# Optimization experiments

Measured on AMD Instinct MI355X. Metric: run time of the kernel, lower is better.

## Reference

```python
import jax, jax.numpy as jnp
import numpy as np

N_GRAPHS = 1250
NEG_SLOPE = 0.2

def gat_layer(x, src, dst, W, a_src, a_dst, b, concat):
    # x: [N, Fin]; W: [Fin, H*C]; a_src/a_dst: [H, C]; b: [H*C] or [C]
    N = x.shape[0]
    H, C = a_src.shape
    h = (x @ W).reshape(N, H, C)                      # [N,H,C]
    alpha_s = jnp.sum(h * a_src[None], axis=-1)       # [N,H]
    alpha_d = jnp.sum(h * a_dst[None], axis=-1)       # [N,H]
    e = jax.nn.leaky_relu(alpha_s[src] + alpha_d[dst], NEG_SLOPE)  # [E,H]
    # segment softmax over incoming edges of each target node
    m = jax.ops.segment_max(e, dst, num_segments=N)   # [N,H]
    m = jnp.where(jnp.isfinite(m), m, 0.0)
    ex = jnp.exp(e - m[dst])
    s = jax.ops.segment_sum(ex, dst, num_segments=N)  # [N,H]
    alpha = ex / (s[dst] + 1e-16)                     # [E,H]
    msg = h[src] * alpha[..., None]                   # [E,H,C]
    out = jax.ops.segment_sum(msg, dst, num_segments=N)  # [N,H,C]
    out = out.reshape(N, H * C) if concat else out.mean(axis=1)
    return out + b

def setup_inputs() -> dict:
    key = jax.random.key(0)
    ks = jax.random.split(key, 13)
    N, E = 50000, 100000
    x = jax.random.normal(ks[0], (N, 78), dtype=jnp.float32)
    edge_index = jax.random.randint(ks[1], (2, E), 0, N, dtype=jnp.int64)
    # sorted segment ids -> every graph non-empty (~40 nodes each)
    batch = jnp.sort(jax.random.randint(ks[2], (N,), 0, N_GRAPHS, dtype=jnp.int64))
    g = lambda k, shape, fan: jax.random.normal(k, shape, dtype=jnp.float32) / np.float32(np.sqrt(fan))
    return {
        'x': x, 'edge_index': edge_index, 'batch': batch,
        'W1': g(ks[3], (78, 780), 78), 'a_src1': g(ks[4], (10, 78), 78), 'a_dst1': g(ks[5], (10, 78), 78),
        'b1': jnp.zeros((780,), jnp.float32),
        'W2': g(ks[6], (780, 128), 780), 'a_src2': g(ks[7], (1, 128), 128), 'a_dst2': g(ks[8], (1, 128), 128),
        'b2': jnp.zeros((128,), jnp.float32),
        'fc_w': g(ks[9], (128, 128), 128), 'fc_b': jnp.zeros((128,), jnp.float32),
    }

def reference(x, edge_index, batch, W1, a_src1, a_dst1, b1, W2, a_src2, a_dst2, b2, fc_w, fc_b):
    N = x.shape[0]
    loop = jnp.arange(N, dtype=edge_index.dtype)
    src = jnp.concatenate([edge_index[0], loop])  # add self loops (PyG default)
    dst = jnp.concatenate([edge_index[1], loop])
    # dropout layers are identity in eval mode
    h = jax.nn.elu(gat_layer(x, src, dst, W1, a_src1, a_dst1, b1, concat=True))   # [N,780]
    h = jax.nn.relu(gat_layer(h, src, dst, W2, a_src2, a_dst2, b2, concat=True))  # [N,128]
    g = jax.ops.segment_max(h, batch, num_segments=N_GRAPHS)                      # [G,128]
    g = jnp.where(jnp.isfinite(g), g, 0.0)
    return jax.nn.relu(g @ fc_w + fc_b)
```

## Files before the change

kernel.cpp:

```cpp
#include <hip/hip_runtime.h>
#include <hip/hip_bf16.h>
#include <cstdint>

#define CAP 32
typedef __hip_bfloat16 bf16;
typedef __attribute__((ext_vector_type(8))) short short8;
typedef __attribute__((ext_vector_type(4))) float f32x4;

__device__ __forceinline__ float sb2f(short s) {
  unsigned int u = ((unsigned int)(unsigned short)s) << 16;
  return __uint_as_float(u);
}
__device__ __forceinline__ short f2sb(float f) {
  bf16 h = __float2bfloat16(f);
  return *reinterpret_cast<short*>(&h);
}

__global__ void k_zero(float* __restrict__ p, int n) {
  int i = blockIdx.x * 256 + threadIdx.x;
  if (i < n) p[i] = 0.f;
}

__global__ void k_detect(const int* __restrict__ ei, int* __restrict__ flag) {
  __shared__ int any;
  if (threadIdx.x == 0) any = 0;
  __syncthreads();
  int v = 0;
  for (int i = 1 + 2 * threadIdx.x; i < 2000; i += 512) v |= ei[i];
  if (v) atomicOr(&any, 1);
  __syncthreads();
  if (threadIdx.x == 0) flag[0] = (any == 0) ? 1 : 0;
}

__device__ __forceinline__ void edge_sd(const int* __restrict__ ei, int e, int f,
                                        int& src, int& dst) {
  if (e < 100000) {
    if (f) { src = ei[2 * e]; dst = ei[200000 + 2 * e]; }
    else   { src = ei[e];     dst = ei[100000 + e]; }
  } else { src = dst = e - 100000; }
  src = min(max(src, 0), 49999);
  dst = min(max(dst, 0), 49999);
}

__global__ void k_prep(const float* __restrict__ x, const float* __restrict__ W1,
                       const float* __restrict__ W2, const float* __restrict__ aw1,
                       const float* __restrict__ dw1, bf16* __restrict__ xb,
                       bf16* __restrict__ W1t, bf16* __restrict__ W2t,
                       bf16* __restrict__ Wat) {
  int i = blockIdx.x * 256 + threadIdx.x;
  const int n_xb = 50000 * 96;
  const int n_w1 = 832 * 96;
  const int n_w2 = 128 * 832;
  const int n_wa = 32 * 96;
  if (i < n_xb) {
    int r = i / 96, k = i - r * 96;
    xb[i] = __float2bfloat16(k < 78 ? x[r * 78 + k] : 0.f);
  } else if (i < n_xb + n_w1) {
    int j = i - n_xb;
    int n = j / 96, k = j - n * 96;
    W1t[j] = __float2bfloat16((k < 78 && n < 780) ? W1[k * 780 + n] : 0.f);
  } else if (i < n_xb + n_w1 + n_w2) {
    int j = i - n_xb - n_w1;
    int c = j / 832, k = j - c * 832;
    W2t[j] = __float2bfloat16(k < 780 ? W2[k * 128 + c] : 0.f);
  } else if (i < n_xb + n_w1 + n_w2 + n_wa) {
    int j = i - n_xb - n_w1 - n_w2;
    int c = j / 96, k = j - c * 96;
    float s = 0.f;
    if (k < 78 && c < 20) {
      const float* w = (c < 10) ? aw1 : dw1;
      int h = (c < 10) ? c : c - 10;
      const float* wrow = W1 + k * 780 + h * 78;
      const float* arow = w + h * 78;
      for (int q = 0; q < 78; q++) s += wrow[q] * arow[q];
    }
    Wat[c * 96 + k] = __float2bfloat16(s);
  }
}

__global__ __launch_bounds__(256) void k_gemm1(const bf16* __restrict__ xb,
                                               const bf16* __restrict__ W1t,
                                               const bf16* __restrict__ Wat,
                                               bf16* __restrict__ H1,
                                               float* __restrict__ as1,
                                               float* __restrict__ ad1) {
  __shared__ __align__(16) short Als[64 * 104];
  __shared__ __align__(16) short Bls[64 * 104];
  __shared__ __align__(16) short Wls[32 * 104];
  const int t = threadIdx.x;
  const int w = t >> 6, l = t & 63, l15 = l & 15, q = l >> 4;
  const int rowBase = blockIdx.x * 64;
  for (int s = t; s < 768; s += 256) {
    int row = s / 12, kg = s - row * 12;
    short8 v = {};
    int gr = rowBase + row;
    if (gr < 50000) v = *(const short8*)((const short*)xb + (size_t)gr * 96 + kg * 8);
    *(short8*)&Als[row * 104 + kg * 8] = v;
  }
  for (int s = t; s < 384; s += 256) {
    int row = s / 12, kg = s - row * 12;
    short8 v = *(const short8*)((const short*)Wat + (size_t)row * 96 + kg * 8);
    *(short8*)&Wls[row * 104 + kg * 8] = v;
  }
  for (int cc = 0; cc < 13; cc++) {
    __syncthreads();
    for (int s = t; s < 768; s += 256) {
      int n = s / 12, kg = s - n * 12;
      short8 v = *(const short8*)((const short*)W1t + (size_t)(cc * 64 + n) * 96 + kg * 8);
      *(short8*)&Bls[n * 104 + kg * 8] = v;
    }
    __syncthreads();
    f32x4 acc[4] = {};
#pragma unroll
    for (int ks = 0; ks < 3; ks++) {
      short8 a = *(const short8*)&Als[(w * 16 + l15) * 104 + ks * 32 + q * 8];
#pragma unroll
      for (int nt = 0; nt < 4; nt++) {
        short8 b = *(const short8*)&Bls[(nt * 16 + l15) * 104 + ks * 32 + q * 8];
        acc[nt] = __builtin_amdgcn_mfma_f32_16x16x32_bf16(a, b, acc[nt], 0, 0, 0);
      }
    }
    const int gr0 = rowBase + w * 16 + q * 4;
#pragma unroll
    for (int nt = 0; nt < 4; nt++) {
      int gc = cc * 64 + nt * 16 + l15;
#pragma unroll
      for (int r = 0; r < 4; r++) {
        int gr = gr0 + r;
        if (gr < 50000) H1[(size_t)gr * 832 + gc] = __float2bfloat16(acc[nt][r]);
      }
    }
  }
  f32x4 acc2[2] = {};
#pragma unroll
  for (int ks = 0; ks < 3; ks++) {
    short8 a = *(const short8*)&Als[(w * 16 + l15) * 104 + ks * 32 + q * 8];
#pragma unroll
    for (int nt = 0; nt < 2; nt++) {
      short8 b = *(const short8*)&Wls[(nt * 16 + l15) * 104 + ks * 32 + q * 8];
      acc2[nt] = __builtin_amdgcn_mfma_f32_16x16x32_bf16(a, b, acc2[nt], 0, 0, 0);
    }
  }
  const int gr0 = rowBase + w * 16 + q * 4;
#pragma unroll
  for (int nt = 0; nt < 2; nt++) {
    int c = nt * 16 + l15;
#pragma unroll
    for (int r = 0; r < 4; r++) {
      int gr = gr0 + r;
      if (gr < 50000) {
        if (c < 10)       as1[gr * 10 + c] = acc2[nt][r];
        else if (c < 20)  ad1[gr * 10 + (c - 10)] = acc2[nt][r];
      }
    }
  }
}

__global__ void k_scatter(const int* __restrict__ ei, const int* __restrict__ flag,
                          int* __restrict__ cnt, int* __restrict__ csr) {
  int e = blockIdx.x * 256 + threadIdx.x;
  if (e >= 150000) return;
  int f = flag[0], src, dst;
  edge_sd(ei, e, f, src, dst);
  int pos = atomicAdd(&cnt[dst], 1);
  if (pos < CAP) csr[dst * CAP + pos] = src;
}

__global__ __launch_bounds__(256) void k_agg1(const bf16* __restrict__ H1,
                                              const float* __restrict__ as1,
                                              const float* __restrict__ ad1,
                                              const int* __restrict__ csr,
                                              const int* __restrict__ cnt,
                                              const float* __restrict__ b1,
                                              bf16* __restrict__ HL2) {
  __shared__ float sexw[2][CAP * 10];
  __shared__ float sden[2][16];
  __shared__ float b1p[832];
  __shared__ int ssrc[2][CAP];
  __shared__ int scnt[2];
  const int t = threadIdx.x;
  const int sub = t >> 7, tt = t & 127;
  const int n = blockIdx.x * 2 + sub;
  if (t < 2) scnt[t] = min(cnt[blockIdx.x * 2 + t], CAP);
  if (t >= 32 && t < 64) { int z = t - 32; sden[z >> 4][z & 15] = 0.f; }
  for (int i = t; i < 832; i += 256) b1p[i] = (i < 780) ? b1[i] : 0.f;
  __syncthreads();
  const int cn = scnt[sub];
  if (tt < cn) ssrc[sub][tt] = csr[n * CAP + tt];
  __syncthreads();
  for (int wv = tt; wv < cn * 10; wv += 128) {
    int k = wv / 10, h = wv - k * 10;
    int src = ssrc[sub][k];
    float e = as1[src * 10 + h] + ad1[n * 10 + h];
    e = e >= 0.f ? e : 0.2f * e;
    float ex = __expf(e);
    sexw[sub][wv] = ex;
    atomicAdd(&sden[sub][h], ex);
  }
  __syncthreads();
  for (int wv = tt; wv < cn * 10; wv += 128) {
    int h = wv % 10;
    sexw[sub][wv] = sexw[sub][wv] / (sden[sub][h] + 1e-16f);
  }
  __syncthreads();
  if (tt < 104) {
    int hj[8];
#pragma unroll
    for (int c = 0; c < 8; c++) {
      int j = tt * 8 + c;
      int h = j / 78;
      hj[c] = h > 9 ? 9 : h;
    }
    float acc[8] = {};
    const float* sw = sexw[sub];
    const short* H1s = (const short*)H1;
    for (int k = 0; k < cn; k++) {
      int src = ssrc[sub][k];
      short8 hv = *(const short8*)(H1s + (size_t)src * 832 + tt * 8);
      const float* swk = sw + k * 10;
#pragma unroll
      for (int c = 0; c < 8; c++) acc[c] += swk[hj[c]] * sb2f(hv[c]);
    }
    short8 ov;
#pragma unroll
    for (int c = 0; c < 8; c++) {
      int j = tt * 8 + c;
      float v = acc[c] + b1p[j];
      v = v > 0.f ? v : __expf(v) - 1.f;
      ov[c] = f2sb(v);
    }
    *(short8*)((short*)HL2 + (size_t)n * 832 + tt * 8) = ov;
  }
}

__global__ __launch_bounds__(256) void k_gemm2(const bf16* __restrict__ A,
                                               const bf16* __restrict__ W2t,
                                               const float* __restrict__ AW2,
                                               const float* __restrict__ DW2,
                                               bf16* __restrict__ H2,
                                               float* __restrict__ as2,
                                               float* __restrict__ ad2) {
  __shared__ __align__(16) short Als[64 * 72];
  __shared__ __align__(16) short Bls[128 * 72];
  __shared__ float sAW[128], sDW[128];
  __shared__ float sS[4][64], sD[4][64];
  const int t = threadIdx.x;
  const int w = t >> 6, l = t & 63, l15 = l & 15, q = l >> 4;
  const int rowBase = blockIdx.x * 64;
  if (t < 128) sAW[t] = AW2[t];
  else         sDW[t - 128] = DW2[t - 128];
  f32x4 acc[4][2] = {};
  for (int kb = 0; kb < 832; kb += 64) {
    __syncthreads();
    for (int s = t; s < 512; s += 256) {
      int row = s >> 3, kg = s & 7;
      short8 v = {};
      int gr = rowBase + row;
      if (gr < 50000) v = *(const short8*)((const short*)A + (size_t)gr * 832 + kb + kg * 8);
      *(short8*)&Als[row * 72 + kg * 8] = v;
    }
    for (int s = t; s < 1024; s += 256) {
      int col = s >> 3, kg = s & 7;
      short8 v = *(const short8*)((const short*)W2t + (size_t)col * 832 + kb + kg * 8);
      *(short8*)&Bls[col * 72 + kg * 8] = v;
    }
    __syncthreads();
#pragma unroll
    for (int ks = 0; ks < 2; ks++) {
      short8 a[4];
#pragma unroll
      for (int mt = 0; mt < 4; mt++)
        a[mt] = *(const short8*)&Als[(mt * 16 + l15) * 72 + ks * 32 + q * 8];
#pragma unroll
      for (int ntl = 0; ntl < 2; ntl++) {
        short8 b = *(const short8*)&Bls[((w * 2 + ntl) * 16 + l15) * 72 + ks * 32 + q * 8];
#pragma unroll
        for (int mt = 0; mt < 4; mt++)
          acc[mt][ntl] = __builtin_amdgcn_mfma_f32_16x16x32_bf16(a[mt], b, acc[mt][ntl], 0, 0, 0);
      }
    }
  }
  const int col0 = w * 32 + l15, col1 = col0 + 16;
  const float aw0 = sAW[col0], aw1 = sAW[col1];
  const float dw0 = sDW[col0], dw1 = sDW[col1];
  f32x4 sp[4], dp[4];
#pragma unroll
  for (int mt = 0; mt < 4; mt++) {
    sp[mt] = acc[mt][0] * aw0 + acc[mt][1] * aw1;
    dp[mt] = acc[mt][0] * dw0 + acc[mt][1] * dw1;
  }
#pragma unroll
  for (int m = 1; m < 16; m <<= 1) {
#pragma unroll
    for (int mt = 0; mt < 4; mt++)
#pragma unroll
      for (int r = 0; r < 4; r++) {
        sp[mt][r] += __shfl_xor(sp[mt][r], m, 64);
        dp[mt][r] += __shfl_xor(dp[mt][r], m, 64);
      }
  }
  if (l15 == 0) {
#pragma unroll
    for (int mt = 0; mt < 4; mt++)
#pragma unroll
      for (int r = 0; r < 4; r++) {
        sS[w][mt * 16 + q * 4 + r] = sp[mt][r];
        sD[w][mt * 16 + q * 4 + r] = dp[mt][r];
      }
  }
#pragma unroll
  for (int mt = 0; mt < 4; mt++) {
    int gr0 = rowBase + mt * 16 + q * 4;
#pragma unroll
    for (int ntl = 0; ntl < 2; ntl++) {
      int gc = w * 32 + ntl * 16 + l15;
#pragma unroll
      for (int r = 0; r < 4; r++) {
        int gr = gr0 + r;
        if (gr < 50000) H2[(size_t)gr * 128 + gc] = __float2bfloat16(acc[mt][ntl][r]);
      }
    }
  }
  __syncthreads();
  if (t < 64) {
    int gr = rowBase + t;
    if (gr < 50000) as2[gr] = sS[0][t] + sS[1][t] + sS[2][t] + sS[3][t];
  } else if (t < 128) {
    int r2 = t - 64;
    int gr = rowBase + r2;
    if (gr < 50000) ad2[gr] = sD[0][r2] + sD[1][r2] + sD[2][r2] + sD[3][r2];
  }
}

__global__ __launch_bounds__(256) void k_agg2(const bf16* __restrict__ H2,
                                              const float* __restrict__ as2,
                                              const float* __restrict__ ad2,
                                              const int* __restrict__ csr,
                                              const int* __restrict__ cnt,
                                              const float* __restrict__ b2,
                                              const int* __restrict__ batch,
                                              const int* __restrict__ flag,
                                              float* __restrict__ g) {
  __shared__ int ssrc[2][CAP];
  __shared__ float sexw[2][CAP];
  __shared__ float sden[2];
  __shared__ int scnt[2], sb[2];
  const int t = threadIdx.x;
  const int sub = t >> 7, tt = t & 127;
  const int n = blockIdx.x * 2 + sub;
  if (t < 2) {
    int nt2 = blockIdx.x * 2 + t;
    scnt[t] = min(cnt[nt2], CAP);
    sden[t] = 0.f;
    int b = flag[0] ? batch[2 * nt2] : batch[nt2];
    sb[t] = min(max(b, 0), 1249);
  }
  __syncthreads();
  const int cn = scnt[sub];
  if (tt < cn) {
    int src = csr[n * CAP + tt];
    ssrc[sub][tt] = src;
    float e = as2[src] + ad2[n];
    e = e >= 0.f ? e : 0.2f * e;
    float ex = __expf(e);
    sexw[sub][tt] = ex;
    atomicAdd(&sden[sub], ex);
  }
  __syncthreads();
  if (tt < cn) sexw[sub][tt] = sexw[sub][tt] / (sden[sub] + 1e-16f);
  __syncthreads();
  const short* H2s = (const short*)H2;
  float acc = 0.f;
  for (int k = 0; k < cn; k++)
    acc += sexw[sub][k] * sb2f(H2s[(size_t)ssrc[sub][k] * 128 + tt]);
  float v = acc + b2[tt];
  v = v > 0.f ? v : 0.f;
  atomicMax((int*)&g[sb[sub] * 128 + tt], __float_as_int(v));
}

__global__ __launch_bounds__(128) void k_fc(const float* __restrict__ g,
                                            const float* __restrict__ fw,
                                            const float* __restrict__ fb,
                                            float* __restrict__ out) {
  const int n = blockIdx.x, t = threadIdx.x;
  __shared__ float grow[128];
  grow[t] = g[n * 128 + t];
  __syncthreads();
  float acc = fb[t];
  for (int k = 0; k < 128; k++) acc += grow[k] * fw[k * 128 + t];
  out[n * 128 + t] = acc > 0.f ? acc : 0.f;
}

extern "C" void kernel_launch(void* const* d_in, const int* in_sizes, int n_in,
                              void* d_out, int out_size, void* d_ws, size_t ws_size,
                              hipStream_t stream) {
  const float* x     = (const float*)d_in[0];
  const int*   ei    = (const int*)d_in[1];
  const int*   batch = (const int*)d_in[2];
  const float* W1    = (const float*)d_in[3];
  const float* as1w  = (const float*)d_in[4];
  const float* ad1w  = (const float*)d_in[5];
  const float* b1    = (const float*)d_in[6];
  const float* W2    = (const float*)d_in[7];
  const float* as2w  = (const float*)d_in[8];
  const float* ad2w  = (const float*)d_in[9];
  const float* b2    = (const float*)d_in[10];
  const float* fcw   = (const float*)d_in[11];
  const float* fcb   = (const float*)d_in[12];
  float* out = (float*)d_out;

  char* p = (char*)d_ws;
  size_t off = 0;
  auto alloc = [&](size_t bytes) -> void* {
    void* r = p + off;
    off = (off + bytes + 15) & ~(size_t)15;
    return r;
  };
  int*   cnt = (int*)  alloc(50000 * 4);
  float* g   = (float*)alloc(160000 * 4);
  size_t zeroWords = off / 4;
  float* as1 = (float*)alloc(500000 * 4);
  float* ad1 = (float*)alloc(500000 * 4);
  float* as2 = (float*)alloc(50000 * 4);
  float* ad2 = (float*)alloc(50000 * 4);
  bf16*  W1t = (bf16*) alloc((size_t)832 * 96 * 2);
  bf16*  W2t = (bf16*) alloc((size_t)128 * 832 * 2);
  bf16*  Wat = (bf16*) alloc((size_t)32 * 96 * 2);
  bf16*  h1  = (bf16*) alloc((size_t)50000 * 832 * 2);
  bf16*  hl2 = (bf16*) alloc((size_t)50000 * 832 * 2);
  int*   csr = (int*)  alloc((size_t)50000 * CAP * 4);
  void*  uni = alloc((size_t)50000 * 128 * 2);
  bf16*  xb  = (bf16*)uni;
  bf16*  h2  = (bf16*)uni;
  int*   flag = (int*) alloc(16);
  (void)ws_size; (void)in_sizes; (void)n_in; (void)out_size;

  k_zero<<<((int)zeroWords + 255) / 256, 256, 0, stream>>>((float*)d_ws, (int)zeroWords);
  k_detect<<<1, 256, 0, stream>>>(ei, flag);
  k_prep<<<(50000 * 96 + 832 * 96 + 128 * 832 + 32 * 96 + 255) / 256, 256, 0, stream>>>(
      x, W1, W2, as1w, ad1w, xb, W1t, W2t, Wat);

  k_gemm1<<<782, 256, 0, stream>>>(xb, W1t, Wat, h1, as1, ad1);
  k_scatter<<<(150000 + 255) / 256, 256, 0, stream>>>(ei, flag, cnt, csr);
  k_agg1<<<25000, 256, 0, stream>>>(h1, as1, ad1, csr, cnt, b1, hl2);
  k_gemm2<<<782, 256, 0, stream>>>(hl2, W2t, as2w, ad2w, h2, as2, ad2);
  k_agg2<<<25000, 256, 0, stream>>>(h2, as2, ad2, csr, cnt, b2, batch, flag, g);
  k_fc<<<1250, 128, 0, stream>>>(g, fcw, fcb, out);
}
```

Before: 320.6 us.

## Prefetch GEMM tiles into registers, stage GEMM1 output via LDS, fold zeroing into prep

Both GEMM kernels now load the next K or N tile from global memory into registers while the current tile is computed, so global latency overlaps with MFMA work. GEMM1 writes its accumulator tile to shared memory first and then stores H1 with coalesced 16-byte bf16 rows instead of scattered 2-byte stores. The separate zeroing kernel is merged into the prep kernel, removing one launch. This costs extra registers and LDS (a 17 KB fp32 staging buffer) plus two extra barriers per chunk, which may lower occupancy. The merge also relies on the prep grid covering at least as many threads as there are words to zero.

```diff
diff --git a/kernel.cpp b/kernel.cpp
--- a/kernel.cpp
+++ b/kernel.cpp
@@ -14,11 +14,6 @@
 __device__ __forceinline__ short f2sb(float f) {
   bf16 h = __float2bfloat16(f);
   return *reinterpret_cast<short*>(&h);
-}
-
-__global__ void k_zero(float* __restrict__ p, int n) {
-  int i = blockIdx.x * 256 + threadIdx.x;
-  if (i < n) p[i] = 0.f;
 }
 
 __global__ void k_detect(const int* __restrict__ ei, int* __restrict__ flag) {
@@ -46,8 +41,9 @@
                        const float* __restrict__ W2, const float* __restrict__ aw1,
                        const float* __restrict__ dw1, bf16* __restrict__ xb,
                        bf16* __restrict__ W1t, bf16* __restrict__ W2t,
-                       bf16* __restrict__ Wat) {
+                       bf16* __restrict__ Wat, float* __restrict__ zp, int zeroWords) {
   int i = blockIdx.x * 256 + threadIdx.x;
+  if (i < zeroWords) zp[i] = 0.f;
   const int n_xb = 50000 * 96;
   const int n_w1 = 832 * 96;
   const int n_w2 = 128 * 832;
@@ -87,6 +83,7 @@
   __shared__ __align__(16) short Als[64 * 104];
   __shared__ __align__(16) short Bls[64 * 104];
   __shared__ __align__(16) short Wls[32 * 104];
+  __shared__ __align__(16) float Cls[64 * 68];
   const int t = threadIdx.x;
   const int w = t >> 6, l = t & 63, l15 = l & 15, q = l >> 4;
   const int rowBase = blockIdx.x * 64;
@@ -99,15 +96,26 @@
   }
   for (int s = t; s < 384; s += 256) {
     int row = s / 12, kg = s - row * 12;
-    short8 v = *(const short8*)((const short*)Wat + (size_t)row * 96 + kg * 8);
-    *(short8*)&Wls[row * 104 + kg * 8] = v;
+    *(short8*)&Wls[row * 104 + kg * 8] =
+        *(const short8*)((const short*)Wat + (size_t)row * 96 + kg * 8);
+  }
+  short8 breg[3];
+  int bn[3], bk[3];
+#pragma unroll
+  for (int i = 0; i < 3; i++) {
+    int s = t + i * 256;
+    bn[i] = s / 12; bk[i] = s - bn[i] * 12;
+    breg[i] = *(const short8*)((const short*)W1t + (size_t)bn[i] * 96 + bk[i] * 8);
   }
   for (int cc = 0; cc < 13; cc++) {
     __syncthreads();
-    for (int s = t; s < 768; s += 256) {
-      int n = s / 12, kg = s - n * 12;
-      short8 v = *(const short8*)((const short*)W1t + (size_t)(cc * 64 + n) * 96 + kg * 8);
-      *(short8*)&Bls[n * 104 + kg * 8] = v;
+#pragma unroll
+    for (int i = 0; i < 3; i++) *(short8*)&Bls[bn[i] * 104 + bk[i] * 8] = breg[i];
+    if (cc < 12) {
+#pragma unroll
+      for (int i = 0; i < 3; i++)
+        breg[i] = *(const short8*)((const short*)W1t +
+                                   (size_t)((cc + 1) * 64 + bn[i]) * 96 + bk[i] * 8);
     }
     __syncthreads();
     f32x4 acc[4] = {};
@@ -120,14 +128,25 @@
         acc[nt] = __builtin_amdgcn_mfma_f32_16x16x32_bf16(a, b, acc[nt], 0, 0, 0);
       }
     }
-    const int gr0 = rowBase + w * 16 + q * 4;
-#pragma unroll
-    for (int nt = 0; nt < 4; nt++) {
-      int gc = cc * 64 + nt * 16 + l15;
-#pragma unroll
-      for (int r = 0; r < 4; r++) {
-        int gr = gr0 + r;
-        if (gr < 50000) H1[(size_t)gr * 832 + gc] = __float2bfloat16(acc[nt][r]);
+    __syncthreads();
+#pragma unroll
+    for (int nt = 0; nt < 4; nt++)
+#pragma unroll
+      for (int r = 0; r < 4; r++)
+        Cls[(w * 16 + q * 4 + r) * 68 + nt * 16 + l15] = acc[nt][r];
+    __syncthreads();
+    {
+      int r = t >> 2, c0 = (t & 3) * 16;
+      int gr = rowBase + r;
+      if (gr < 50000) {
+        short8 o0, o1;
+#pragma unroll
+        for (int c = 0; c < 8; c++) o0[c] = f2sb(Cls[r * 68 + c0 + c]);
+#pragma unroll
+        for (int c = 0; c < 8; c++) o1[c] = f2sb(Cls[r * 68 + c0 + 8 + c]);
+        short* dst = (short*)H1 + (size_t)gr * 832 + cc * 64 + c0;
+        *(short8*)dst = o0;
+        *(short8*)(dst + 8) = o1;
       }
     }
   }
@@ -249,20 +268,54 @@
   const int rowBase = blockIdx.x * 64;
   if (t < 128) sAW[t] = AW2[t];
   else         sDW[t - 128] = DW2[t - 128];
+  const int ar = t >> 2, ak = t & 3;
+  const int bc = t >> 1, bk2 = t & 1;
+  short8 areg[2], breg[4];
+  {
+    int gr0 = rowBase + ar;
+#pragma unroll
+    for (int i = 0; i < 2; i++) {
+      short8 v = {};
+      int gr = gr0;
+      if (gr < 50000)
+        v = *(const short8*)((const short*)A + (size_t)gr * 832 + 0 + (ak * 2 + i) * 8);
+      areg[i] = v;
+    }
+#pragma unroll
+    for (int i = 0; i < 4; i++) {
+      int s = t + i * 256;
+      int col = s >> 3, kg = s & 7;
+      breg[i] = *(const short8*)((const short*)W2t + (size_t)col * 832 + 0 + kg * 8);
+    }
+  }
   f32x4 acc[4][2] = {};
   for (int kb = 0; kb < 832; kb += 64) {
     __syncthreads();
-    for (int s = t; s < 512; s += 256) {
-      int row = s >> 3, kg = s & 7;
-      short8 v = {};
-      int gr = rowBase + row;
-      if (gr < 50000) v = *(const short8*)((const short*)A + (size_t)gr * 832 + kb + kg * 8);
-      *(short8*)&Als[row * 72 + kg * 8] = v;
-    }
-    for (int s = t; s < 1024; s += 256) {
+#pragma unroll
+    for (int i = 0; i < 2; i++)
+      *(short8*)&Als[ar * 72 + (ak * 2 + i) * 8] = areg[i];
+#pragma unroll
+    for (int i = 0; i < 4; i++) {
+      int s = t + i * 256;
       int col = s >> 3, kg = s & 7;
-      short8 v = *(const short8*)((const short*)W2t + (size_t)col * 832 + kb + kg * 8);
-      *(short8*)&Bls[col * 72 + kg * 8] = v;
+      *(short8*)&Bls[col * 72 + kg * 8] = breg[i];
+    }
+    if (kb < 768) {
+      int kn = kb + 64;
+      int gr = rowBase + ar;
+#pragma unroll
+      for (int i = 0; i < 2; i++) {
+        short8 v = {};
+        if (gr < 50000)
+          v = *(const short8*)((const short*)A + (size_t)gr * 832 + kn + (ak * 2 + i) * 8);
+        areg[i] = v;
+      }
+#pragma unroll
+      for (int i = 0; i < 4; i++) {
+        int s = t + i * 256;
+        int col = s >> 3, kg = s & 7;
+        breg[i] = *(const short8*)((const short*)W2t + (size_t)col * 832 + kn + kg * 8);
+      }
     }
     __syncthreads();
 #pragma unroll
@@ -435,10 +488,10 @@
   int*   flag = (int*) alloc(16);
   (void)ws_size; (void)in_sizes; (void)n_in; (void)out_size;
 
-  k_zero<<<((int)zeroWords + 255) / 256, 256, 0, stream>>>((float*)d_ws, (int)zeroWords);
   k_detect<<<1, 256, 0, stream>>>(ei, flag);
-  k_prep<<<(50000 * 96 + 832 * 96 + 128 * 832 + 32 * 96 + 255) / 256, 256, 0, stream>>>(
-      x, W1, W2, as1w, ad1w, xb, W1t, W2t, Wat);
+  int prepN = 50000 * 96 + 832 * 96 + 128 * 832 + 32 * 96;
+  k_prep<<<(prepN + 255) / 256, 256, 0, stream>>>(
+      x, W1, W2, as1w, ad1w, xb, W1t, W2t, Wat, (float*)d_ws, (int)zeroWords);
 
   k_gemm1<<<782, 256, 0, stream>>>(xb, W1t, Wat, h1, as1, ad1);
   k_scatter<<<(150000 + 255) / 256, 256, 0, stream>>>(ei, flag, cnt, csr);
```

Result: faster. 294.2 us (-8.2%).

## Aggregate raw inputs before layer-1 projection and fuse projection into layer-2 GEMM

Applied to the files above, without the earlier changes.

The layer-1 GEMM that materialised the N×780 hidden tensor is dropped. Attention-weighted aggregation now runs on the 78-wide inputs per head, giving a 10×96 aggregate per node. A fused kernel then applies each head's block of W1, the bias and ELU in shared memory, and feeds the result straight into the layer-2 GEMM. This removes a large intermediate write and re-read and shrinks the gather width in aggregation, at the cost of a per-node 10-head aggregate buffer and more MFMA work per GEMM block. Zeroing moves into the prep kernel, and the separate normalisation passes and metadata syncs in the aggregation kernels are removed.

```diff
diff --git a/kernel.cpp b/kernel.cpp
--- a/kernel.cpp
+++ b/kernel.cpp
@@ -14,11 +14,6 @@
 __device__ __forceinline__ short f2sb(float f) {
   bf16 h = __float2bfloat16(f);
   return *reinterpret_cast<short*>(&h);
-}
-
-__global__ void k_zero(float* __restrict__ p, int n) {
-  int i = blockIdx.x * 256 + threadIdx.x;
-  if (i < n) p[i] = 0.f;
 }
 
 __global__ void k_detect(const int* __restrict__ ei, int* __restrict__ flag) {
@@ -45,26 +40,19 @@
 __global__ void k_prep(const float* __restrict__ x, const float* __restrict__ W1,
                        const float* __restrict__ W2, const float* __restrict__ aw1,
                        const float* __restrict__ dw1, bf16* __restrict__ xb,
-                       bf16* __restrict__ W1t, bf16* __restrict__ W2t,
-                       bf16* __restrict__ Wat) {
+                       bf16* __restrict__ Wat, bf16* __restrict__ W1bdp,
+                       bf16* __restrict__ W2h, float* __restrict__ zp, int zeroWords) {
   int i = blockIdx.x * 256 + threadIdx.x;
+  if (i < zeroWords) zp[i] = 0.f;
   const int n_xb = 50000 * 96;
-  const int n_w1 = 832 * 96;
-  const int n_w2 = 128 * 832;
   const int n_wa = 32 * 96;
+  const int n_bd = 10 * 96 * 96;
+  const int n_w2 = 10 * 128 * 96;
   if (i < n_xb) {
     int r = i / 96, k = i - r * 96;
     xb[i] = __float2bfloat16(k < 78 ? x[r * 78 + k] : 0.f);
-  } else if (i < n_xb + n_w1) {
+  } else if (i < n_xb + n_wa) {
     int j = i - n_xb;
-    int n = j / 96, k = j - n * 96;
-    W1t[j] = __float2bfloat16((k < 78 && n < 780) ? W1[k * 780 + n] : 0.f);
-  } else if (i < n_xb + n_w1 + n_w2) {
-    int j = i - n_xb - n_w1;
-    int c = j / 832, k = j - c * 832;
-    W2t[j] = __float2bfloat16(k < 780 ? W2[k * 128 + c] : 0.f);
-  } else if (i < n_xb + n_w1 + n_w2 + n_wa) {
-    int j = i - n_xb - n_w1 - n_w2;
     int c = j / 96, k = j - c * 96;
     float s = 0.f;
     if (k < 78 && c < 20) {
@@ -75,17 +63,26 @@
       for (int q = 0; q < 78; q++) s += wrow[q] * arow[q];
     }
     Wat[c * 96 + k] = __float2bfloat16(s);
-  }
-}
-
-__global__ __launch_bounds__(256) void k_gemm1(const bf16* __restrict__ xb,
-                                               const bf16* __restrict__ W1t,
+  } else if (i < n_xb + n_wa + n_bd) {
+    int j = i - n_xb - n_wa;
+    int hh = j / 9216;
+    int rem = j - hh * 9216;
+    int jj = rem / 96, k = rem - jj * 96;
+    W1bdp[j] = __float2bfloat16((jj < 78 && k < 78) ? W1[k * 780 + hh * 78 + jj] : 0.f);
+  } else if (i < n_xb + n_wa + n_bd + n_w2) {
+    int j = i - n_xb - n_wa - n_bd;
+    int hh = j / 12288;
+    int rem = j - hh * 12288;
+    int c = rem / 96, k = rem - c * 96;
+    W2h[j] = __float2bfloat16(k < 78 ? W2[(hh * 78 + k) * 128 + c] : 0.f);
+  }
+}
+
+__global__ __launch_bounds__(256) void k_alpha(const bf16* __restrict__ xb,
                                                const bf16* __restrict__ Wat,
-                                               bf16* __restrict__ H1,
                                                float* __restrict__ as1,
                                                float* __restrict__ ad1) {
   __shared__ __align__(16) short Als[64 * 104];
-  __shared__ __align__(16) short Bls[64 * 104];
   __shared__ __align__(16) short Wls[32 * 104];
   const int t = threadIdx.x;
   const int w = t >> 6, l = t & 63, l15 = l & 15, q = l >> 4;
@@ -99,38 +96,10 @@
   }
   for (int s = t; s < 384; s += 256) {
     int row = s / 12, kg = s - row * 12;
-    short8 v = *(const short8*)((const short*)Wat + (size_t)row * 96 + kg * 8);
-    *(short8*)&Wls[row * 104 + kg * 8] = v;
-  }
-  for (int cc = 0; cc < 13; cc++) {
-    __syncthreads();
-    for (int s = t; s < 768; s += 256) {
-      int n = s / 12, kg = s - n * 12;
-      short8 v = *(const short8*)((const short*)W1t + (size_t)(cc * 64 + n) * 96 + kg * 8);
-      *(short8*)&Bls[n * 104 + kg * 8] = v;
-    }
-    __syncthreads();
-    f32x4 acc[4] = {};
-#pragma unroll
-    for (int ks = 0; ks < 3; ks++) {
-      short8 a = *(const short8*)&Als[(w * 16 + l15) * 104 + ks * 32 + q * 8];
-#pragma unroll
-      for (int nt = 0; nt < 4; nt++) {
-        short8 b = *(const short8*)&Bls[(nt * 16 + l15) * 104 + ks * 32 + q * 8];
-        acc[nt] = __builtin_amdgcn_mfma_f32_16x16x32_bf16(a, b, acc[nt], 0, 0, 0);
-      }
-    }
-    const int gr0 = rowBase + w * 16 + q * 4;
-#pragma unroll
-    for (int nt = 0; nt < 4; nt++) {
-      int gc = cc * 64 + nt * 16 + l15;
-#pragma unroll
-      for (int r = 0; r < 4; r++) {
-        int gr = gr0 + r;
-        if (gr < 50000) H1[(size_t)gr * 832 + gc] = __float2bfloat16(acc[nt][r]);
-      }
-    }
-  }
+    *(short8*)&Wls[row * 104 + kg * 8] =
+        *(const short8*)((const short*)Wat + (size_t)row * 96 + kg * 8);
+  }
+  __syncthreads();
   f32x4 acc2[2] = {};
 #pragma unroll
   for (int ks = 0; ks < 3; ks++) {
@@ -166,26 +135,20 @@
   if (pos < CAP) csr[dst * CAP + pos] = src;
 }
 
-__global__ __launch_bounds__(256) void k_agg1(const bf16* __restrict__ H1,
+__global__ __launch_bounds__(256) void k_aggx(const bf16* __restrict__ xb,
                                               const float* __restrict__ as1,
                                               const float* __restrict__ ad1,
                                               const int* __restrict__ csr,
                                               const int* __restrict__ cnt,
-                                              const float* __restrict__ b1,
-                                              bf16* __restrict__ HL2) {
+                                              bf16* __restrict__ aggx) {
   __shared__ float sexw[2][CAP * 10];
   __shared__ float sden[2][16];
-  __shared__ float b1p[832];
   __shared__ int ssrc[2][CAP];
-  __shared__ int scnt[2];
   const int t = threadIdx.x;
   const int sub = t >> 7, tt = t & 127;
   const int n = blockIdx.x * 2 + sub;
-  if (t < 2) scnt[t] = min(cnt[blockIdx.x * 2 + t], CAP);
-  if (t >= 32 && t < 64) { int z = t - 32; sden[z >> 4][z & 15] = 0.f; }
-  for (int i = t; i < 832; i += 256) b1p[i] = (i < 780) ? b1[i] : 0.f;
-  __syncthreads();
-  const int cn = scnt[sub];
+  if (tt < 16) sden[sub][tt] = 0.f;
+  const int cn = min(cnt[n], CAP);
   if (tt < cn) ssrc[sub][tt] = csr[n * CAP + tt];
   __syncthreads();
   for (int wv = tt; wv < cn * 10; wv += 128) {
@@ -198,82 +161,102 @@
     atomicAdd(&sden[sub][h], ex);
   }
   __syncthreads();
-  for (int wv = tt; wv < cn * 10; wv += 128) {
-    int h = wv % 10;
-    sexw[sub][wv] = sexw[sub][wv] / (sden[sub][h] + 1e-16f);
-  }
-  __syncthreads();
-  if (tt < 104) {
-    int hj[8];
-#pragma unroll
-    for (int c = 0; c < 8; c++) {
-      int j = tt * 8 + c;
-      int h = j / 78;
-      hj[c] = h > 9 ? 9 : h;
-    }
-    float acc[8] = {};
-    const float* sw = sexw[sub];
-    const short* H1s = (const short*)H1;
+  if (tt < 96) {
+    float acc[10];
+#pragma unroll
+    for (int h = 0; h < 10; h++) acc[h] = 0.f;
+    const short* xs = (const short*)xb;
     for (int k = 0; k < cn; k++) {
       int src = ssrc[sub][k];
-      short8 hv = *(const short8*)(H1s + (size_t)src * 832 + tt * 8);
-      const float* swk = sw + k * 10;
-#pragma unroll
-      for (int c = 0; c < 8; c++) acc[c] += swk[hj[c]] * sb2f(hv[c]);
-    }
-    short8 ov;
-#pragma unroll
-    for (int c = 0; c < 8; c++) {
-      int j = tt * 8 + c;
-      float v = acc[c] + b1p[j];
-      v = v > 0.f ? v : __expf(v) - 1.f;
-      ov[c] = f2sb(v);
-    }
-    *(short8*)((short*)HL2 + (size_t)n * 832 + tt * 8) = ov;
-  }
-}
-
-__global__ __launch_bounds__(256) void k_gemm2(const bf16* __restrict__ A,
-                                               const bf16* __restrict__ W2t,
-                                               const float* __restrict__ AW2,
-                                               const float* __restrict__ DW2,
-                                               bf16* __restrict__ H2,
-                                               float* __restrict__ as2,
-                                               float* __restrict__ ad2) {
-  __shared__ __align__(16) short Als[64 * 72];
-  __shared__ __align__(16) short Bls[128 * 72];
-  __shared__ float sAW[128], sDW[128];
+      float xv = sb2f(xs[(size_t)src * 96 + tt]);
+      const float* swk = sexw[sub] + k * 10;
+#pragma unroll
+      for (int h = 0; h < 10; h++) acc[h] += swk[h] * xv;
+    }
+    short* outp = (short*)aggx + (size_t)n * 960 + tt;
+#pragma unroll
+    for (int h = 0; h < 10; h++)
+      outp[h * 96] = f2sb(acc[h] / (sden[sub][h] + 1e-16f));
+  }
+}
+
+__global__ __launch_bounds__(256) void k_gemm2f(const bf16* __restrict__ aggx,
+                                                const bf16* __restrict__ W1bdp,
+                                                const bf16* __restrict__ W2h,
+                                                const float* __restrict__ b1,
+                                                const float* __restrict__ AW2,
+                                                const float* __restrict__ DW2,
+                                                bf16* __restrict__ H2,
+                                                float* __restrict__ as2,
+                                                float* __restrict__ ad2) {
+  __shared__ __align__(16) short Ain[64 * 104];
+  __shared__ __align__(16) short Ah[64 * 104];
+  __shared__ __align__(16) short Bw[96 * 104];
+  __shared__ __align__(16) short Bls[128 * 104];
+  __shared__ float sb1[784];
   __shared__ float sS[4][64], sD[4][64];
   const int t = threadIdx.x;
   const int w = t >> 6, l = t & 63, l15 = l & 15, q = l >> 4;
   const int rowBase = blockIdx.x * 64;
-  if (t < 128) sAW[t] = AW2[t];
-  else         sDW[t - 128] = DW2[t - 128];
+  for (int i = t; i < 784; i += 256) sb1[i] = (i < 780) ? b1[i] : 0.f;
   f32x4 acc[4][2] = {};
-  for (int kb = 0; kb < 832; kb += 64) {
+  for (int h = 0; h < 10; h++) {
     __syncthreads();
-    for (int s = t; s < 512; s += 256) {
-      int row = s >> 3, kg = s & 7;
+#pragma unroll
+    for (int i = 0; i < 3; i++) {
+      int s = t + i * 256;
+      int row = s / 12, kg = s - row * 12;
+      int gr = rowBase + row;
       short8 v = {};
-      int gr = rowBase + row;
-      if (gr < 50000) v = *(const short8*)((const short*)A + (size_t)gr * 832 + kb + kg * 8);
-      *(short8*)&Als[row * 72 + kg * 8] = v;
-    }
-    for (int s = t; s < 1024; s += 256) {
-      int col = s >> 3, kg = s & 7;
-      short8 v = *(const short8*)((const short*)W2t + (size_t)col * 832 + kb + kg * 8);
-      *(short8*)&Bls[col * 72 + kg * 8] = v;
+      if (gr < 50000)
+        v = *(const short8*)((const short*)aggx + ((size_t)gr * 10 + h) * 96 + kg * 8);
+      *(short8*)&Ain[row * 104 + kg * 8] = v;
+    }
+    for (int s = t; s < 1152; s += 256) {
+      int row = s / 12, kg = s - row * 12;
+      *(short8*)&Bw[row * 104 + kg * 8] =
+          *(const short8*)((const short*)W1bdp + (size_t)h * 9216 + row * 96 + kg * 8);
+    }
+#pragma unroll
+    for (int i = 0; i < 6; i++) {
+      int s = t + i * 256;
+      int col = s / 12, kg = s - col * 12;
+      *(short8*)&Bls[col * 104 + kg * 8] =
+          *(const short8*)((const short*)W2h + (size_t)h * 12288 + col * 96 + kg * 8);
     }
     __syncthreads();
-#pragma unroll
-    for (int ks = 0; ks < 2; ks++) {
+    f32x4 cacc[6] = {};
+#pragma unroll
+    for (int ks = 0; ks < 3; ks++) {
+      short8 a = *(const short8*)&Ain[(w * 16 + l15) * 104 + ks * 32 + q * 8];
+#pragma unroll
+      for (int nt = 0; nt < 6; nt++) {
+        short8 b = *(const short8*)&Bw[(nt * 16 + l15) * 104 + ks * 32 + q * 8];
+        cacc[nt] = __builtin_amdgcn_mfma_f32_16x16x32_bf16(a, b, cacc[nt], 0, 0, 0);
+      }
+    }
+#pragma unroll
+    for (int nt = 0; nt < 6; nt++) {
+      int col = nt * 16 + l15;
+      float bb = (col < 78) ? sb1[h * 78 + col] : 0.f;
+#pragma unroll
+      for (int r = 0; r < 4; r++) {
+        int row = w * 16 + q * 4 + r;
+        float v = cacc[nt][r] + bb;
+        v = v > 0.f ? v : __expf(v) - 1.f;
+        Ah[row * 104 + col] = f2sb(v);
+      }
+    }
+    __syncthreads();
+#pragma unroll
+    for (int ks = 0; ks < 3; ks++) {
       short8 a[4];
 #pragma unroll
       for (int mt = 0; mt < 4; mt++)
-        a[mt] = *(const short8*)&Als[(mt * 16 + l15) * 72 + ks * 32 + q * 8];
+        a[mt] = *(const short8*)&Ah[(mt * 16 + l15) * 104 + ks * 32 + q * 8];
 #pragma unroll
       for (int ntl = 0; ntl < 2; ntl++) {
-        short8 b = *(const short8*)&Bls[((w * 2 + ntl) * 16 + l15) * 72 + ks * 32 + q * 8];
+        short8 b = *(const short8*)&Bls[((w * 2 + ntl) * 16 + l15) * 104 + ks * 32 + q * 8];
 #pragma unroll
         for (int mt = 0; mt < 4; mt++)
           acc[mt][ntl] = __builtin_amdgcn_mfma_f32_16x16x32_bf16(a[mt], b, acc[mt][ntl], 0, 0, 0);
@@ -281,8 +264,8 @@
     }
   }
   const int col0 = w * 32 + l15, col1 = col0 + 16;
-  const float aw0 = sAW[col0], aw1 = sAW[col1];
-  const float dw0 = sDW[col0], dw1 = sDW[col1];
+  const float aw0 = AW2[col0], aw1 = AW2[col1];
+  const float dw0 = DW2[col0], dw1 = DW2[col1];
   f32x4 sp[4], dp[4];
 #pragma unroll
   for (int mt = 0; mt < 4; mt++) {
@@ -344,19 +327,12 @@
   __shared__ int ssrc[2][CAP];
   __shared__ float sexw[2][CAP];
   __shared__ float sden[2];
-  __shared__ int scnt[2], sb[2];
   const int t = threadIdx.x;
   const int sub = t >> 7, tt = t & 127;
   const int n = blockIdx.x * 2 + sub;
-  if (t < 2) {
-    int nt2 = blockIdx.x * 2 + t;
-    scnt[t] = min(cnt[nt2], CAP);
-    sden[t] = 0.f;
-    int b = flag[0] ? batch[2 * nt2] : batch[nt2];
-    sb[t] = min(max(b, 0), 1249);
-  }
-  __syncthreads();
-  const int cn = scnt[sub];
+  if (tt == 0) sden[sub] = 0.f;
+  __syncthreads();
+  const int cn = min(cnt[n], CAP);
   if (tt < cn) {
     int src = csr[n * CAP + tt];
     ssrc[sub][tt] = src;
@@ -367,15 +343,15 @@
     atomicAdd(&sden[sub], ex);
   }
   __syncthreads();
-  if (tt < cn) sexw[sub][tt] = sexw[sub][tt] / (sden[sub] + 1e-16f);
-  __syncthreads();
   const short* H2s = (const short*)H2;
   float acc = 0.f;
   for (int k = 0; k < cn; k++)
     acc += sexw[sub][k] * sb2f(H2s[(size_t)ssrc[sub][k] * 128 + tt]);
-  float v = acc + b2[tt];
+  float v = acc / (sden[sub] + 1e-16f) + b2[tt];
   v = v > 0.f ? v : 0.f;
-  atomicMax((int*)&g[sb[sub] * 128 + tt], __float_as_int(v));
+  int b = flag[0] ? batch[2 * n] : batch[n];
+  b = min(max(b, 0), 1249);
+  atomicMax((int*)&g[b * 128 + tt], __float_as_int(v));
 }
 
 __global__ __launch_bounds__(128) void k_fc(const float* __restrict__ g,
@@ -419,31 +395,30 @@
   int*   cnt = (int*)  alloc(50000 * 4);
   float* g   = (float*)alloc(160000 * 4);
   size_t zeroWords = off / 4;
-  float* as1 = (float*)alloc(500000 * 4);
-  float* ad1 = (float*)alloc(500000 * 4);
-  float* as2 = (float*)alloc(50000 * 4);
-  float* ad2 = (float*)alloc(50000 * 4);
-  bf16*  W1t = (bf16*) alloc((size_t)832 * 96 * 2);
-  bf16*  W2t = (bf16*) alloc((size_t)128 * 832 * 2);
-  bf16*  Wat = (bf16*) alloc((size_t)32 * 96 * 2);
-  bf16*  h1  = (bf16*) alloc((size_t)50000 * 832 * 2);
-  bf16*  hl2 = (bf16*) alloc((size_t)50000 * 832 * 2);
-  int*   csr = (int*)  alloc((size_t)50000 * CAP * 4);
+  float* as1   = (float*)alloc(500000 * 4);
+  float* ad1   = (float*)alloc(500000 * 4);
+  float* as2   = (float*)alloc(50000 * 4);
+  float* ad2   = (float*)alloc(50000 * 4);
+  bf16*  Wat   = (bf16*) alloc((size_t)32 * 96 * 2);
+  bf16*  W1bdp = (bf16*) alloc((size_t)10 * 96 * 96 * 2);
+  bf16*  W2h   = (bf16*) alloc((size_t)10 * 128 * 96 * 2);
+  bf16*  aggx  = (bf16*) alloc((size_t)50000 * 10 * 96 * 2);
+  int*   csr   = (int*)  alloc((size_t)50000 * CAP * 4);
   void*  uni = alloc((size_t)50000 * 128 * 2);
   bf16*  xb  = (bf16*)uni;
   bf16*  h2  = (bf16*)uni;
   int*   flag = (int*) alloc(16);
   (void)ws_size; (void)in_sizes; (void)n_in; (void)out_size;
 
-  k_zero<<<((int)zeroWords + 255) / 256, 256, 0, stream>>>((float*)d_ws, (int)zeroWords);
   k_detect<<<1, 256, 0, stream>>>(ei, flag);
-  k_prep<<<(50000 * 96 + 832 * 96 + 128 * 832 + 32 * 96 + 255) / 256, 256, 0, stream>>>(
-      x, W1, W2, as1w, ad1w, xb, W1t, W2t, Wat);
-
-  k_gemm1<<<782, 256, 0, stream>>>(xb, W1t, Wat, h1, as1, ad1);
+  int prepN = 50000 * 96 + 32 * 96 + 10 * 96 * 96 + 10 * 128 * 96;
+  k_prep<<<(prepN + 255) / 256, 256, 0, stream>>>(
+      x, W1, W2, as1w, ad1w, xb, Wat, W1bdp, W2h, (float*)d_ws, (int)zeroWords);
+
+  k_alpha<<<782, 256, 0, stream>>>(xb, Wat, as1, ad1);
   k_scatter<<<(150000 + 255) / 256, 256, 0, stream>>>(ei, flag, cnt, csr);
-  k_agg1<<<25000, 256, 0, stream>>>(h1, as1, ad1, csr, cnt, b1, hl2);
-  k_gemm2<<<782, 256, 0, stream>>>(hl2, W2t, as2w, ad2w, h2, as2, ad2);
+  k_aggx<<<25000, 256, 0, stream>>>(xb, as1, ad1, csr, cnt, aggx);
+  k_gemm2f<<<782, 256, 0, stream>>>(aggx, W1bdp, W2h, b1, as2w, ad2w, h2, as2, ad2);
   k_agg2<<<25000, 256, 0, stream>>>(h2, as2, ad2, csr, cnt, b2, batch, flag, g);
   k_fc<<<1250, 128, 0, stream>>>(g, fcw, fcb, out);
 }
```

After: 298.9 us. 1.07x faster.
